# Performance work log

Hardware: AMD Instinct MI355X
Metric: run time of the kernel (lower is better)

The kernel has to match this reference:

```python
import jax, jax.numpy as jnp
import numpy as np

N_GRAPHS, NODES_PER, DEG, D = 128, 1024, 32, 256
N = N_GRAPHS * NODES_PER          # 131072 nodes
E = N * DEG                       # 4194304 edges
RATIO = 0.8
K = int(np.ceil(RATIO * NODES_PER))  # 820 nodes kept per graph


def setup_inputs() -> dict:
    key = jax.random.key(0)
    k1, k2, k3, k4 = jax.random.split(key, 4)
    x = jax.random.normal(k1, (N, D), dtype=jnp.float32)
    # intra-graph random edges: endpoints within [0, NODES_PER) + graph offset
    src = jax.random.randint(k2, (E,), 0, NODES_PER)
    dst = jax.random.randint(k3, (E,), 0, NODES_PER)
    goff = (jnp.arange(E) // (NODES_PER * DEG)) * NODES_PER
    edge_index = jnp.stack([src + goff, dst + goff]).astype(jnp.int32)
    batch = jnp.repeat(jnp.arange(N_GRAPHS, dtype=jnp.int32), NODES_PER)
    W = jax.random.normal(k4, (D, 1), dtype=jnp.float32) / np.sqrt(D)
    b = jnp.zeros((1,), dtype=jnp.float32)
    return {"x": x, "edge_index": edge_index, "batch": batch, "W": W, "b": b}


def _gcn_score(x, edge_index, W, b):
    # GCNConv(in_channels, 1) with added self-loops and symmetric normalization
    n = x.shape[0]
    row, col = edge_index[0], edge_index[1]  # source, target
    # degree at target, init 1.0 accounts for self-loop
    deg = jnp.ones((n,), x.dtype).at[col].add(jnp.ones_like(col, dtype=x.dtype))
    dinv = jax.lax.rsqrt(deg)
    h = x @ W                                 # [n, 1]
    norm = dinv[row] * dinv[col]              # [E]
    agg = jnp.zeros_like(h).at[col].add(norm[:, None] * h[row])
    agg = agg + (dinv * dinv)[:, None] * h    # self-loop contribution deg^-1 * h_i
    return (agg + b).squeeze(-1)              # [n]


def reference(x, edge_index, batch, W, b):
    score = _gcn_score(x, edge_index, W, b)                     # [N]
    # per-graph top-k (graphs are contiguous, equal size)
    score_g = score.reshape(N_GRAPHS, NODES_PER)
    _, idx = jax.lax.top_k(score_g, K)                          # [G, K]
    perm = (idx + jnp.arange(N_GRAPHS)[:, None] * NODES_PER).reshape(-1)  # [G*K]
    x_new = x[perm] * jnp.tanh(score[perm])[:, None]            # [G*K, D]
    batch_new = batch[perm]
    # filter_adj: remap kept nodes to new ids, mask edges with dropped endpoints
    new_id = jnp.full((x.shape[0],), -1, dtype=perm.dtype).at[perm].set(
        jnp.arange(perm.shape[0], dtype=perm.dtype))
    r2 = new_id[edge_index[0]]
    c2 = new_id[edge_index[1]]
    edge_mask = (r2 >= 0) & (c2 >= 0)                           # [E] valid edges
    edge_index_new = jnp.where(edge_mask, jnp.stack([r2, c2]), -1)  # [2, E], -1 = dropped
    return x_new, edge_index_new, edge_mask, batch_new, perm
```

## Files before the change

### kernel.cpp

```cpp
#include <hip/hip_runtime.h>
#include <math.h>

constexpr int NG    = 128;
constexpr int NP    = 1024;
constexpr int D     = 256;
constexpr int NTOT  = NG * NP;
constexpr int EPG   = NP * 32;
constexpr int ET    = NTOT * 32;
constexpr int KK    = 820;
constexpr int NKEEP = NG * KK;
constexpr int BPG   = 4;
constexpr int EPB   = EPG / BPG;
constexpr int NBE   = NG * BPG;

constexpr long long OUT_X     = 0;
constexpr long long OUT_EI0   = (long long)NKEEP * D;
constexpr long long OUT_EI1   = OUT_EI0 + ET;
constexpr long long OUT_MASK  = OUT_EI0 + 2LL * ET;
constexpr long long OUT_BATCH = OUT_MASK + ET;
constexpr long long OUT_PERM  = OUT_BATCH + NKEEP;

__global__ void node_init_kernel(const float* __restrict__ x,
                                 const float* __restrict__ W,
                                 float* __restrict__ h,
                                 int* __restrict__ new_id) {
    int row  = blockIdx.x * 4 + (threadIdx.x >> 6);
    int lane = threadIdx.x & 63;
    float4 a = ((const float4*)(x + (size_t)row * D))[lane];
    float4 w = ((const float4*)W)[lane];
    float s = a.x * w.x + a.y * w.y + a.z * w.z + a.w * w.w;
#pragma unroll
    for (int off = 32; off > 0; off >>= 1) s += __shfl_down(s, off, 64);
    if (lane == 0) {
        h[row]      = s;
        new_id[row] = -1;
    }
}

__global__ __launch_bounds__(256) void deg_part_kernel(const int* __restrict__ cols,
                                                       int* __restrict__ deg_part) {
    __shared__ int cnt[NP];
    const int b = blockIdx.x;
    const int g = b >> 2;
    for (int i = threadIdx.x; i < NP; i += 256) cnt[i] = 0;
    __syncthreads();
    const int4* c4 = (const int4*)(cols + (size_t)g * EPG + (size_t)(b & 3) * EPB);
#pragma unroll
    for (int i = threadIdx.x; i < EPB / 4; i += 256) {
        int4 c = c4[i];
        atomicAdd(&cnt[c.x & (NP - 1)], 1);
        atomicAdd(&cnt[c.y & (NP - 1)], 1);
        atomicAdd(&cnt[c.z & (NP - 1)], 1);
        atomicAdd(&cnt[c.w & (NP - 1)], 1);
    }
    __syncthreads();
    int* dst = deg_part + (size_t)b * NP;
    for (int i = threadIdx.x; i < NP; i += 256) dst[i] = cnt[i];
}

__global__ __launch_bounds__(256) void acc_part_kernel(const int* __restrict__ rows,
                                                       const int* __restrict__ cols,
                                                       const float* __restrict__ h,
                                                       const int* __restrict__ deg_part,
                                                       float* __restrict__ acc_part) {
    __shared__ float ul[NP];
    __shared__ float acc[NP];
    const int b = blockIdx.x;
    const int g = b >> 2;
    const int* dp = deg_part + (size_t)g * BPG * NP;
    for (int i = threadIdx.x; i < NP; i += 256) {
        int d = 1 + dp[i] + dp[NP + i] + dp[2 * NP + i] + dp[3 * NP + i];
        ul[i]  = rsqrtf((float)d) * h[g * NP + i];
        acc[i] = 0.0f;
    }
    __syncthreads();
    size_t eoff = (size_t)g * EPG + (size_t)(b & 3) * EPB;
    const int4* c4 = (const int4*)(cols + eoff);
    const int4* r4 = (const int4*)(rows + eoff);
#pragma unroll
    for (int i = threadIdx.x; i < EPB / 4; i += 256) {
        int4 c = c4[i];
        int4 r = r4[i];
        atomicAdd(&acc[c.x & (NP - 1)], ul[r.x & (NP - 1)]);
        atomicAdd(&acc[c.y & (NP - 1)], ul[r.y & (NP - 1)]);
        atomicAdd(&acc[c.z & (NP - 1)], ul[r.z & (NP - 1)]);
        atomicAdd(&acc[c.w & (NP - 1)], ul[r.w & (NP - 1)]);
    }
    __syncthreads();
    float* dst = acc_part + (size_t)b * NP;
    for (int i = threadIdx.x; i < NP; i += 256) dst[i] = acc[i];
}

__global__ __launch_bounds__(1024) void sort_kernel(
        const float* __restrict__ h, const float* __restrict__ b,
        const int* __restrict__ deg_part, const float* __restrict__ acc_part,
        int* __restrict__ perm_i, int* __restrict__ new_id,
        float* __restrict__ factor,
        float* __restrict__ out_perm, float* __restrict__ out_batch) {
    __shared__ unsigned long long sk[NP];
    __shared__ float scl[NP];

    const int g = blockIdx.x;
    const int t = threadIdx.x;
    const int*   dp = deg_part + (size_t)g * BPG * NP;
    const float* ap = acc_part + (size_t)g * BPG * NP;

    int   d  = 1 + dp[t] + dp[NP + t] + dp[2 * NP + t] + dp[3 * NP + t];
    float av = ap[t] + ap[NP + t] + ap[2 * NP + t] + ap[3 * NP + t];
    float hv = h[g * NP + t];
    float di = rsqrtf((float)d);
    float score = di * av + di * di * hv + b[0];
    scl[t] = score;

    unsigned int fu = __float_as_uint(score);
    unsigned int s  = (fu & 0x80000000u) ? ~fu : (fu | 0x80000000u);
    unsigned long long key = ((unsigned long long)(~s) << 32) | (unsigned int)t;

    for (int k = 2; k <= NP; k <<= 1) {
        for (int j = k >> 1; j > 0; j >>= 1) {
            unsigned long long other;
            if (j < 64) {
                other = __shfl_xor(key, j, 64);
            } else {
                sk[t] = key;
                __syncthreads();
                other = sk[t ^ j];
                __syncthreads();
            }
            bool take_min = (((t & k) == 0) == ((t & j) == 0));
            bool omin = other < key;
            key = (take_min == omin) ? other : key;
        }
    }

    if (t < KK) {
        int idx  = (int)(key & 0xFFFFFFFFull);
        int node = g * NP + idx;
        int j    = g * KK + t;
        perm_i[j]    = node;
        new_id[node] = j;
        out_perm[j]  = (float)node;
        out_batch[j] = (float)g;
        factor[j]    = tanhf(scl[idx]);
    }
}

__global__ void gather_kernel(const float* __restrict__ x,
                              const int* __restrict__ perm_i,
                              const float* __restrict__ factor,
                              float* __restrict__ out_x) {
    int j    = blockIdx.x * 4 + (threadIdx.x >> 6);
    int lane = threadIdx.x & 63;
    int node = perm_i[j];
    float t  = factor[j];
    float4 v = ((const float4*)(x + (size_t)node * D))[lane];
    float4 o = make_float4(v.x * t, v.y * t, v.z * t, v.w * t);
    ((float4*)(out_x + (size_t)j * D))[lane] = o;
}

__global__ __launch_bounds__(256) void edge_kernel(const int* __restrict__ rows,
                                                   const int* __restrict__ cols,
                                                   const int* __restrict__ new_id,
                                                   float* __restrict__ out_r,
                                                   float* __restrict__ out_c,
                                                   float* __restrict__ out_m) {
    __shared__ int nid[NP];
    const int b = blockIdx.x;
    const int g = b >> 2;
    for (int i = threadIdx.x; i < NP; i += 256) nid[i] = new_id[g * NP + i];
    __syncthreads();
    size_t eoff = (size_t)g * EPG + (size_t)(b & 3) * EPB;
    const int4* r4 = (const int4*)(rows + eoff);
    const int4* c4 = (const int4*)(cols + eoff);
    float4* orr = (float4*)(out_r + eoff);
    float4* occ = (float4*)(out_c + eoff);
    float4* omm = (float4*)(out_m + eoff);
#pragma unroll
    for (int i = threadIdx.x; i < EPB / 4; i += 256) {
        int4 r = r4[i];
        int4 c = c4[i];
        float4 fr, fc, fm;
        {
            int nr = nid[r.x & (NP - 1)], nc = nid[c.x & (NP - 1)];
            bool m = (nr >= 0) && (nc >= 0);
            fr.x = m ? (float)nr : -1.0f; fc.x = m ? (float)nc : -1.0f; fm.x = m ? 1.0f : 0.0f;
        }
        {
            int nr = nid[r.y & (NP - 1)], nc = nid[c.y & (NP - 1)];
            bool m = (nr >= 0) && (nc >= 0);
            fr.y = m ? (float)nr : -1.0f; fc.y = m ? (float)nc : -1.0f; fm.y = m ? 1.0f : 0.0f;
        }
        {
            int nr = nid[r.z & (NP - 1)], nc = nid[c.z & (NP - 1)];
            bool m = (nr >= 0) && (nc >= 0);
            fr.z = m ? (float)nr : -1.0f; fc.z = m ? (float)nc : -1.0f; fm.z = m ? 1.0f : 0.0f;
        }
        {
            int nr = nid[r.w & (NP - 1)], nc = nid[c.w & (NP - 1)];
            bool m = (nr >= 0) && (nc >= 0);
            fr.w = m ? (float)nr : -1.0f; fc.w = m ? (float)nc : -1.0f; fm.w = m ? 1.0f : 0.0f;
        }
        orr[i] = fr;
        occ[i] = fc;
        omm[i] = fm;
    }
}

extern "C" void kernel_launch(void* const* d_in, const int* in_sizes, int n_in,
                              void* d_out, int out_size, void* d_ws, size_t ws_size,
                              hipStream_t stream) {
    const float* x  = (const float*)d_in[0];
    const int*   ei = (const int*)d_in[1];
    const float* W  = (const float*)d_in[3];
    const float* b  = (const float*)d_in[4];
    float* out = (float*)d_out;

    float* wsf      = (float*)d_ws;
    float* h        = wsf;
    int*   new_id   = (int*)wsf + NTOT;
    int*   perm_i   = (int*)wsf + 2 * NTOT;
    float* factor   = wsf + 2 * NTOT + NKEEP;
    int*   deg_part = (int*)wsf + 2 * NTOT + 2 * NKEEP;
    float* acc_part = wsf + 2 * NTOT + 2 * NKEEP + NBE * NP;

    const int* rows = ei;
    const int* cols = ei + ET;

    hipLaunchKernelGGL(node_init_kernel, dim3(NTOT / 4), dim3(256), 0, stream,
                       x, W, h, new_id);
    hipLaunchKernelGGL(deg_part_kernel, dim3(NBE), dim3(256), 0, stream,
                       cols, deg_part);
    hipLaunchKernelGGL(acc_part_kernel, dim3(NBE), dim3(256), 0, stream,
                       rows, cols, h, deg_part, acc_part);
    hipLaunchKernelGGL(sort_kernel, dim3(NG), dim3(1024), 0, stream,
                       h, b, deg_part, acc_part, perm_i, new_id, factor,
                       out + OUT_PERM, out + OUT_BATCH);
    hipLaunchKernelGGL(gather_kernel, dim3(NKEEP / 4), dim3(256), 0, stream,
                       x, perm_i, factor, out + OUT_X);
    hipLaunchKernelGGL(edge_kernel, dim3(NBE), dim3(256), 0, stream,
                       rows, cols, new_id, out + OUT_EI0, out + OUT_EI1, out + OUT_MASK);
}
```

Baseline: 335.7 us.

## Fuse all stages into one cooperative persistent kernel with grid syncs

Replaces six separate kernel launches with a single cooperative kernel of 256 blocks of 1024 threads, separated by grid.sync() barriers. Each graph's edges are now split across two blocks instead of four, and node projection and gather are spread over the persistent blocks. The goal is to remove launch overhead and inter-kernel gaps. In exchange, the grid is smaller (256 blocks on a large GPU), there are grid-wide barriers, and only half the blocks do the sort phase, so memory-bound phases may get less parallelism.

```diff
diff --git a/kernel.cpp b/kernel.cpp
--- a/kernel.cpp
+++ b/kernel.cpp
@@ -1,5 +1,8 @@
 #include <hip/hip_runtime.h>
+#include <hip/hip_cooperative_groups.h>
 #include <math.h>
+
+namespace cg = cooperative_groups;
 
 constexpr int NG    = 128;
 constexpr int NP    = 1024;
@@ -9,9 +12,11 @@
 constexpr int ET    = NTOT * 32;
 constexpr int KK    = 820;
 constexpr int NKEEP = NG * KK;
-constexpr int BPG   = 4;
-constexpr int EPB   = EPG / BPG;
-constexpr int NBE   = NG * BPG;
+
+constexpr int NBLK  = 256;
+constexpr int EHALF = EPG / 2;
+constexpr int ROWS_PER_BLK  = NTOT  / NBLK;
+constexpr int GROWS_PER_BLK = NKEEP / NBLK;
 
 constexpr long long OUT_X     = 0;
 constexpr long long OUT_EI0   = (long long)NKEEP * D;
@@ -20,195 +25,187 @@
 constexpr long long OUT_BATCH = OUT_MASK + ET;
 constexpr long long OUT_PERM  = OUT_BATCH + NKEEP;
 
-__global__ void node_init_kernel(const float* __restrict__ x,
-                                 const float* __restrict__ W,
-                                 float* __restrict__ h,
-                                 int* __restrict__ new_id) {
-    int row  = blockIdx.x * 4 + (threadIdx.x >> 6);
-    int lane = threadIdx.x & 63;
-    float4 a = ((const float4*)(x + (size_t)row * D))[lane];
-    float4 w = ((const float4*)W)[lane];
-    float s = a.x * w.x + a.y * w.y + a.z * w.z + a.w * w.w;
-#pragma unroll
-    for (int off = 32; off > 0; off >>= 1) s += __shfl_down(s, off, 64);
-    if (lane == 0) {
-        h[row]      = s;
-        new_id[row] = -1;
-    }
-}
-
-__global__ __launch_bounds__(256) void deg_part_kernel(const int* __restrict__ cols,
-                                                       int* __restrict__ deg_part) {
-    __shared__ int cnt[NP];
-    const int b = blockIdx.x;
-    const int g = b >> 2;
-    for (int i = threadIdx.x; i < NP; i += 256) cnt[i] = 0;
-    __syncthreads();
-    const int4* c4 = (const int4*)(cols + (size_t)g * EPG + (size_t)(b & 3) * EPB);
-#pragma unroll
-    for (int i = threadIdx.x; i < EPB / 4; i += 256) {
-        int4 c = c4[i];
-        atomicAdd(&cnt[c.x & (NP - 1)], 1);
-        atomicAdd(&cnt[c.y & (NP - 1)], 1);
-        atomicAdd(&cnt[c.z & (NP - 1)], 1);
-        atomicAdd(&cnt[c.w & (NP - 1)], 1);
-    }
-    __syncthreads();
-    int* dst = deg_part + (size_t)b * NP;
-    for (int i = threadIdx.x; i < NP; i += 256) dst[i] = cnt[i];
-}
-
-__global__ __launch_bounds__(256) void acc_part_kernel(const int* __restrict__ rows,
-                                                       const int* __restrict__ cols,
-                                                       const float* __restrict__ h,
-                                                       const int* __restrict__ deg_part,
-                                                       float* __restrict__ acc_part) {
-    __shared__ float ul[NP];
-    __shared__ float acc[NP];
-    const int b = blockIdx.x;
-    const int g = b >> 2;
-    const int* dp = deg_part + (size_t)g * BPG * NP;
-    for (int i = threadIdx.x; i < NP; i += 256) {
-        int d = 1 + dp[i] + dp[NP + i] + dp[2 * NP + i] + dp[3 * NP + i];
-        ul[i]  = rsqrtf((float)d) * h[g * NP + i];
-        acc[i] = 0.0f;
-    }
-    __syncthreads();
-    size_t eoff = (size_t)g * EPG + (size_t)(b & 3) * EPB;
-    const int4* c4 = (const int4*)(cols + eoff);
-    const int4* r4 = (const int4*)(rows + eoff);
-#pragma unroll
-    for (int i = threadIdx.x; i < EPB / 4; i += 256) {
-        int4 c = c4[i];
-        int4 r = r4[i];
-        atomicAdd(&acc[c.x & (NP - 1)], ul[r.x & (NP - 1)]);
-        atomicAdd(&acc[c.y & (NP - 1)], ul[r.y & (NP - 1)]);
-        atomicAdd(&acc[c.z & (NP - 1)], ul[r.z & (NP - 1)]);
-        atomicAdd(&acc[c.w & (NP - 1)], ul[r.w & (NP - 1)]);
-    }
-    __syncthreads();
-    float* dst = acc_part + (size_t)b * NP;
-    for (int i = threadIdx.x; i < NP; i += 256) dst[i] = acc[i];
-}
-
-__global__ __launch_bounds__(1024) void sort_kernel(
-        const float* __restrict__ h, const float* __restrict__ b,
-        const int* __restrict__ deg_part, const float* __restrict__ acc_part,
-        int* __restrict__ perm_i, int* __restrict__ new_id,
-        float* __restrict__ factor,
-        float* __restrict__ out_perm, float* __restrict__ out_batch) {
+__global__ __launch_bounds__(1024, 4) void fused_kernel(
+        const float* __restrict__ x,   const int* __restrict__ rows,
+        const int* __restrict__ cols,  const float* __restrict__ W,
+        const float* __restrict__ bptr,
+        float* __restrict__ h,         int* __restrict__ new_id,
+        int* __restrict__ perm_i,      float* __restrict__ factor,
+        int* __restrict__ deg_part,    float* __restrict__ acc_part,
+        float* __restrict__ out) {
+    cg::grid_group grid = cg::this_grid();
+
     __shared__ unsigned long long sk[NP];
     __shared__ float scl[NP];
 
-    const int g = blockIdx.x;
-    const int t = threadIdx.x;
-    const int*   dp = deg_part + (size_t)g * BPG * NP;
-    const float* ap = acc_part + (size_t)g * BPG * NP;
-
-    int   d  = 1 + dp[t] + dp[NP + t] + dp[2 * NP + t] + dp[3 * NP + t];
-    float av = ap[t] + ap[NP + t] + ap[2 * NP + t] + ap[3 * NP + t];
-    float hv = h[g * NP + t];
-    float di = rsqrtf((float)d);
-    float score = di * av + di * di * hv + b[0];
-    scl[t] = score;
-
-    unsigned int fu = __float_as_uint(score);
-    unsigned int s  = (fu & 0x80000000u) ? ~fu : (fu | 0x80000000u);
-    unsigned long long key = ((unsigned long long)(~s) << 32) | (unsigned int)t;
-
-    for (int k = 2; k <= NP; k <<= 1) {
-        for (int j = k >> 1; j > 0; j >>= 1) {
-            unsigned long long other;
-            if (j < 64) {
-                other = __shfl_xor(key, j, 64);
-            } else {
-                sk[t] = key;
-                __syncthreads();
-                other = sk[t ^ j];
-                __syncthreads();
-            }
-            bool take_min = (((t & k) == 0) == ((t & j) == 0));
-            bool omin = other < key;
-            key = (take_min == omin) ? other : key;
-        }
-    }
-
-    if (t < KK) {
-        int idx  = (int)(key & 0xFFFFFFFFull);
-        int node = g * NP + idx;
-        int j    = g * KK + t;
-        perm_i[j]    = node;
-        new_id[node] = j;
-        out_perm[j]  = (float)node;
-        out_batch[j] = (float)g;
-        factor[j]    = tanhf(scl[idx]);
-    }
-}
-
-__global__ void gather_kernel(const float* __restrict__ x,
-                              const int* __restrict__ perm_i,
-                              const float* __restrict__ factor,
-                              float* __restrict__ out_x) {
-    int j    = blockIdx.x * 4 + (threadIdx.x >> 6);
-    int lane = threadIdx.x & 63;
-    int node = perm_i[j];
-    float t  = factor[j];
-    float4 v = ((const float4*)(x + (size_t)node * D))[lane];
-    float4 o = make_float4(v.x * t, v.y * t, v.z * t, v.w * t);
-    ((float4*)(out_x + (size_t)j * D))[lane] = o;
-}
-
-__global__ __launch_bounds__(256) void edge_kernel(const int* __restrict__ rows,
-                                                   const int* __restrict__ cols,
-                                                   const int* __restrict__ new_id,
-                                                   float* __restrict__ out_r,
-                                                   float* __restrict__ out_c,
-                                                   float* __restrict__ out_m) {
-    __shared__ int nid[NP];
-    const int b = blockIdx.x;
-    const int g = b >> 2;
-    for (int i = threadIdx.x; i < NP; i += 256) nid[i] = new_id[g * NP + i];
-    __syncthreads();
-    size_t eoff = (size_t)g * EPG + (size_t)(b & 3) * EPB;
-    const int4* r4 = (const int4*)(rows + eoff);
-    const int4* c4 = (const int4*)(cols + eoff);
-    float4* orr = (float4*)(out_r + eoff);
-    float4* occ = (float4*)(out_c + eoff);
-    float4* omm = (float4*)(out_m + eoff);
-#pragma unroll
-    for (int i = threadIdx.x; i < EPB / 4; i += 256) {
-        int4 r = r4[i];
-        int4 c = c4[i];
-        float4 fr, fc, fm;
-        {
-            int nr = nid[r.x & (NP - 1)], nc = nid[c.x & (NP - 1)];
-            bool m = (nr >= 0) && (nc >= 0);
-            fr.x = m ? (float)nr : -1.0f; fc.x = m ? (float)nc : -1.0f; fm.x = m ? 1.0f : 0.0f;
-        }
-        {
-            int nr = nid[r.y & (NP - 1)], nc = nid[c.y & (NP - 1)];
-            bool m = (nr >= 0) && (nc >= 0);
-            fr.y = m ? (float)nr : -1.0f; fc.y = m ? (float)nc : -1.0f; fm.y = m ? 1.0f : 0.0f;
-        }
-        {
-            int nr = nid[r.z & (NP - 1)], nc = nid[c.z & (NP - 1)];
-            bool m = (nr >= 0) && (nc >= 0);
-            fr.z = m ? (float)nr : -1.0f; fc.z = m ? (float)nc : -1.0f; fm.z = m ? 1.0f : 0.0f;
-        }
-        {
-            int nr = nid[r.w & (NP - 1)], nc = nid[c.w & (NP - 1)];
-            bool m = (nr >= 0) && (nc >= 0);
-            fr.w = m ? (float)nr : -1.0f; fc.w = m ? (float)nc : -1.0f; fm.w = m ? 1.0f : 0.0f;
-        }
-        orr[i] = fr;
-        occ[i] = fc;
-        omm[i] = fm;
+    const int blk  = blockIdx.x;
+    const int t    = threadIdx.x;
+    const int w    = t >> 6;
+    const int lane = t & 63;
+    const int g2   = blk >> 1;
+    const int half = blk & 1;
+
+    {
+        int* cnt = (int*)sk;
+        for (int i = t; i < NP; i += 1024) cnt[i] = 0;
+        __syncthreads();
+
+        float4 w4 = ((const float4*)W)[lane];
+        const int base = blk * ROWS_PER_BLK;
+        for (int r = w; r < ROWS_PER_BLK; r += 16) {
+            const int row = base + r;
+            float4 a = ((const float4*)(x + (size_t)row * D))[lane];
+            float s = a.x * w4.x + a.y * w4.y + a.z * w4.z + a.w * w4.w;
+#pragma unroll
+            for (int off = 32; off > 0; off >>= 1) s += __shfl_down(s, off, 64);
+            if (lane == 0) { h[row] = s; new_id[row] = -1; }
+        }
+
+        const int4* c4 = (const int4*)(cols + (size_t)g2 * EPG + (size_t)half * EHALF);
+#pragma unroll
+        for (int i = t; i < EHALF / 4; i += 1024) {
+            int4 c = c4[i];
+            atomicAdd(&cnt[c.x & (NP - 1)], 1);
+            atomicAdd(&cnt[c.y & (NP - 1)], 1);
+            atomicAdd(&cnt[c.z & (NP - 1)], 1);
+            atomicAdd(&cnt[c.w & (NP - 1)], 1);
+        }
+        __syncthreads();
+        int* dst = deg_part + (size_t)blk * NP;
+        for (int i = t; i < NP; i += 1024) dst[i] = cnt[i];
+    }
+    grid.sync();
+
+    {
+        float* ul  = (float*)sk;
+        float* acc = (float*)sk + NP;
+        const int* dp = deg_part + (size_t)(2 * g2) * NP;
+        for (int i = t; i < NP; i += 1024) {
+            int d  = 1 + dp[i] + dp[NP + i];
+            ul[i]  = rsqrtf((float)d) * h[g2 * NP + i];
+            acc[i] = 0.0f;
+        }
+        __syncthreads();
+        const size_t eo = (size_t)g2 * EPG + (size_t)half * EHALF;
+        const int4* c4 = (const int4*)(cols + eo);
+        const int4* r4 = (const int4*)(rows + eo);
+#pragma unroll
+        for (int i = t; i < EHALF / 4; i += 1024) {
+            int4 c = c4[i];
+            int4 r = r4[i];
+            atomicAdd(&acc[c.x & (NP - 1)], ul[r.x & (NP - 1)]);
+            atomicAdd(&acc[c.y & (NP - 1)], ul[r.y & (NP - 1)]);
+            atomicAdd(&acc[c.z & (NP - 1)], ul[r.z & (NP - 1)]);
+            atomicAdd(&acc[c.w & (NP - 1)], ul[r.w & (NP - 1)]);
+        }
+        __syncthreads();
+        float* dst = acc_part + (size_t)blk * NP;
+        for (int i = t; i < NP; i += 1024) dst[i] = acc[i];
+    }
+    grid.sync();
+
+    if (blk < NG) {
+        const int g = blk;
+        const int*   dp = deg_part + (size_t)(2 * g) * NP;
+        const float* ap = acc_part + (size_t)(2 * g) * NP;
+        int   d  = 1 + dp[t] + dp[NP + t];
+        float av = ap[t] + ap[NP + t];
+        float hv = h[g * NP + t];
+        float di = rsqrtf((float)d);
+        float score = di * av + di * di * hv + bptr[0];
+        scl[t] = score;
+
+        unsigned int fu = __float_as_uint(score);
+        unsigned int s  = (fu & 0x80000000u) ? ~fu : (fu | 0x80000000u);
+        unsigned long long key = ((unsigned long long)(~s) << 32) | (unsigned int)t;
+
+        for (int k = 2; k <= NP; k <<= 1) {
+            for (int j = k >> 1; j > 0; j >>= 1) {
+                unsigned long long other;
+                if (j < 64) {
+                    other = __shfl_xor(key, j, 64);
+                } else {
+                    sk[t] = key;
+                    __syncthreads();
+                    other = sk[t ^ j];
+                    __syncthreads();
+                }
+                bool take_min = (((t & k) == 0) == ((t & j) == 0));
+                bool omin = other < key;
+                key = (take_min == omin) ? other : key;
+            }
+        }
+
+        if (t < KK) {
+            int idx  = (int)(key & 0xFFFFFFFFull);
+            int node = g * NP + idx;
+            int jj   = g * KK + t;
+            perm_i[jj]   = node;
+            new_id[node] = jj;
+            out[OUT_PERM + jj]  = (float)node;
+            out[OUT_BATCH + jj] = (float)g;
+            factor[jj] = tanhf(scl[idx]);
+        }
+    }
+    grid.sync();
+
+    {
+        const int base = blk * GROWS_PER_BLK;
+        for (int r = w; r < GROWS_PER_BLK; r += 16) {
+            const int j    = base + r;
+            const int node = perm_i[j];
+            const float f  = factor[j];
+            float4 v = ((const float4*)(x + (size_t)node * D))[lane];
+            ((float4*)(out + OUT_X + (size_t)j * D))[lane] =
+                make_float4(v.x * f, v.y * f, v.z * f, v.w * f);
+        }
+
+        int* nid = (int*)sk;
+        for (int i = t; i < NP; i += 1024) nid[i] = new_id[g2 * NP + i];
+        __syncthreads();
+        const size_t eo = (size_t)g2 * EPG + (size_t)half * EHALF;
+        const int4* r4 = (const int4*)(rows + eo);
+        const int4* c4 = (const int4*)(cols + eo);
+        float4* orr = (float4*)(out + OUT_EI0  + eo);
+        float4* occ = (float4*)(out + OUT_EI1  + eo);
+        float4* omm = (float4*)(out + OUT_MASK + eo);
+#pragma unroll
+        for (int i = t; i < EHALF / 4; i += 1024) {
+            int4 r = r4[i];
+            int4 c = c4[i];
+            float4 fr, fc, fm;
+            {
+                int nr = nid[r.x & (NP - 1)], nc = nid[c.x & (NP - 1)];
+                bool m = (nr >= 0) && (nc >= 0);
+                fr.x = m ? (float)nr : -1.0f; fc.x = m ? (float)nc : -1.0f; fm.x = m ? 1.0f : 0.0f;
+            }
+            {
+                int nr = nid[r.y & (NP - 1)], nc = nid[c.y & (NP - 1)];
+                bool m = (nr >= 0) && (nc >= 0);
+                fr.y = m ? (float)nr : -1.0f; fc.y = m ? (float)nc : -1.0f; fm.y = m ? 1.0f : 0.0f;
+            }
+            {
+                int nr = nid[r.z & (NP - 1)], nc = nid[c.z & (NP - 1)];
+                bool m = (nr >= 0) && (nc >= 0);
+                fr.z = m ? (float)nr : -1.0f; fc.z = m ? (float)nc : -1.0f; fm.z = m ? 1.0f : 0.0f;
+            }
+            {
+                int nr = nid[r.w & (NP - 1)], nc = nid[c.w & (NP - 1)];
+                bool m = (nr >= 0) && (nc >= 0);
+                fr.w = m ? (float)nr : -1.0f; fc.w = m ? (float)nc : -1.0f; fm.w = m ? 1.0f : 0.0f;
+            }
+            orr[i] = fr;
+            occ[i] = fc;
+            omm[i] = fm;
+        }
     }
 }
 
 extern "C" void kernel_launch(void* const* d_in, const int* in_sizes, int n_in,
                               void* d_out, int out_size, void* d_ws, size_t ws_size,
                               hipStream_t stream) {
+    (void)in_sizes; (void)n_in; (void)out_size; (void)ws_size;
+
     const float* x  = (const float*)d_in[0];
     const int*   ei = (const int*)d_in[1];
     const float* W  = (const float*)d_in[3];
@@ -217,26 +214,18 @@
 
     float* wsf      = (float*)d_ws;
     float* h        = wsf;
-    int*   new_id   = (int*)wsf + NTOT;
-    int*   perm_i   = (int*)wsf + 2 * NTOT;
+    int*   new_id   = (int*)(wsf + NTOT);
+    int*   perm_i   = (int*)(wsf + 2 * NTOT);
     float* factor   = wsf + 2 * NTOT + NKEEP;
-    int*   deg_part = (int*)wsf + 2 * NTOT + 2 * NKEEP;
-    float* acc_part = wsf + 2 * NTOT + 2 * NKEEP + NBE * NP;
+    int*   deg_part = (int*)(wsf + 2 * NTOT + 2 * NKEEP);
+    float* acc_part = wsf + 2 * NTOT + 2 * NKEEP + NBLK * NP;
 
     const int* rows = ei;
     const int* cols = ei + ET;
 
-    hipLaunchKernelGGL(node_init_kernel, dim3(NTOT / 4), dim3(256), 0, stream,
-                       x, W, h, new_id);
-    hipLaunchKernelGGL(deg_part_kernel, dim3(NBE), dim3(256), 0, stream,
-                       cols, deg_part);
-    hipLaunchKernelGGL(acc_part_kernel, dim3(NBE), dim3(256), 0, stream,
-                       rows, cols, h, deg_part, acc_part);
-    hipLaunchKernelGGL(sort_kernel, dim3(NG), dim3(1024), 0, stream,
-                       h, b, deg_part, acc_part, perm_i, new_id, factor,
-                       out + OUT_PERM, out + OUT_BATCH);
-    hipLaunchKernelGGL(gather_kernel, dim3(NKEEP / 4), dim3(256), 0, stream,
-                       x, perm_i, factor, out + OUT_X);
-    hipLaunchKernelGGL(edge_kernel, dim3(NBE), dim3(256), 0, stream,
-                       rows, cols, new_id, out + OUT_EI0, out + OUT_EI1, out + OUT_MASK);
+    void* args[] = { (void*)&x, (void*)&rows, (void*)&cols, (void*)&W, (void*)&b,
+                     (void*)&h, (void*)&new_id, (void*)&perm_i, (void*)&factor,
+                     (void*)&deg_part, (void*)&acc_part, (void*)&out };
+    hipLaunchCooperativeKernel((const void*)fused_kernel, dim3(NBLK), dim3(1024),
+                               args, 0, stream);
 }
```

New measurement: 445.9 us. +32.8%, slower.

## Fuse node projection with degree counting and gather with edge remap kernels

Applied to the files above, without the earlier changes.

Merges the node projection (x@W) kernel with the per-graph degree histogram into one launch, and merges the x gather/scale kernel with the edge remap kernel into another. Both use 2048 blocks: the first 512 do the edge work while every block also processes a strided share of rows, so independent memory-bound streams can overlap within one grid and two launches go away. The cost is that blocks doing edge work carry extra load, and the row loops now run serially per wave instead of one row per wave. There is also no barrier before the x-gather part, which is fine since it does not touch shared memory.

```diff
diff --git a/kernel.cpp b/kernel.cpp
--- a/kernel.cpp
+++ b/kernel.cpp
@@ -13,6 +13,10 @@
 constexpr int EPB   = EPG / BPG;
 constexpr int NBE   = NG * BPG;
 
+constexpr int K1_BLOCKS = 2048;
+constexpr int K4_BLOCKS = 2048;
+constexpr int K1_ROWS_PER_WAVE = NTOT / (K1_BLOCKS * 4);
+
 constexpr long long OUT_X     = 0;
 constexpr long long OUT_EI0   = (long long)NKEEP * D;
 constexpr long long OUT_EI1   = OUT_EI0 + ET;
@@ -20,49 +24,57 @@
 constexpr long long OUT_BATCH = OUT_MASK + ET;
 constexpr long long OUT_PERM  = OUT_BATCH + NKEEP;
 
-__global__ void node_init_kernel(const float* __restrict__ x,
-                                 const float* __restrict__ W,
-                                 float* __restrict__ h,
-                                 int* __restrict__ new_id) {
-    int row  = blockIdx.x * 4 + (threadIdx.x >> 6);
-    int lane = threadIdx.x & 63;
-    float4 a = ((const float4*)(x + (size_t)row * D))[lane];
-    float4 w = ((const float4*)W)[lane];
-    float s = a.x * w.x + a.y * w.y + a.z * w.z + a.w * w.w;
-#pragma unroll
-    for (int off = 32; off > 0; off >>= 1) s += __shfl_down(s, off, 64);
-    if (lane == 0) {
-        h[row]      = s;
-        new_id[row] = -1;
-    }
-}
-
-__global__ __launch_bounds__(256) void deg_part_kernel(const int* __restrict__ cols,
-                                                       int* __restrict__ deg_part) {
+__global__ __launch_bounds__(256) void k1_h_deg(const float* __restrict__ x,
+                                                const float* __restrict__ W,
+                                                const int* __restrict__ cols,
+                                                float* __restrict__ h,
+                                                int* __restrict__ new_id,
+                                                int* __restrict__ deg_part) {
     __shared__ int cnt[NP];
-    const int b = blockIdx.x;
-    const int g = b >> 2;
-    for (int i = threadIdx.x; i < NP; i += 256) cnt[i] = 0;
-    __syncthreads();
-    const int4* c4 = (const int4*)(cols + (size_t)g * EPG + (size_t)(b & 3) * EPB);
-#pragma unroll
-    for (int i = threadIdx.x; i < EPB / 4; i += 256) {
-        int4 c = c4[i];
-        atomicAdd(&cnt[c.x & (NP - 1)], 1);
-        atomicAdd(&cnt[c.y & (NP - 1)], 1);
-        atomicAdd(&cnt[c.z & (NP - 1)], 1);
-        atomicAdd(&cnt[c.w & (NP - 1)], 1);
-    }
-    __syncthreads();
-    int* dst = deg_part + (size_t)b * NP;
-    for (int i = threadIdx.x; i < NP; i += 256) dst[i] = cnt[i];
-}
-
-__global__ __launch_bounds__(256) void acc_part_kernel(const int* __restrict__ rows,
-                                                       const int* __restrict__ cols,
-                                                       const float* __restrict__ h,
-                                                       const int* __restrict__ deg_part,
-                                                       float* __restrict__ acc_part) {
+    const int b    = blockIdx.x;
+    const int t    = threadIdx.x;
+    const int w    = t >> 6;
+    const int lane = t & 63;
+    const bool do_deg = (b < NBE);
+
+    if (do_deg) {
+        for (int i = t; i < NP; i += 256) cnt[i] = 0;
+        __syncthreads();
+    }
+
+    float4 w4 = ((const float4*)W)[lane];
+    const int base = (b * 4 + w) * K1_ROWS_PER_WAVE;
+    for (int r = 0; r < K1_ROWS_PER_WAVE; ++r) {
+        const int row = base + r;
+        float4 a = ((const float4*)(x + (size_t)row * D))[lane];
+        float s = a.x * w4.x + a.y * w4.y + a.z * w4.z + a.w * w4.w;
+#pragma unroll
+        for (int off = 32; off > 0; off >>= 1) s += __shfl_down(s, off, 64);
+        if (lane == 0) { h[row] = s; new_id[row] = -1; }
+    }
+
+    if (do_deg) {
+        const int g = b >> 2;
+        const int4* c4 = (const int4*)(cols + (size_t)g * EPG + (size_t)(b & 3) * EPB);
+#pragma unroll
+        for (int i = t; i < EPB / 4; i += 256) {
+            int4 c = c4[i];
+            atomicAdd(&cnt[c.x & (NP - 1)], 1);
+            atomicAdd(&cnt[c.y & (NP - 1)], 1);
+            atomicAdd(&cnt[c.z & (NP - 1)], 1);
+            atomicAdd(&cnt[c.w & (NP - 1)], 1);
+        }
+        __syncthreads();
+        int* dst = deg_part + (size_t)b * NP;
+        for (int i = t; i < NP; i += 256) dst[i] = cnt[i];
+    }
+}
+
+__global__ __launch_bounds__(256) void k2_acc(const int* __restrict__ rows,
+                                              const int* __restrict__ cols,
+                                              const float* __restrict__ h,
+                                              const int* __restrict__ deg_part,
+                                              float* __restrict__ acc_part) {
     __shared__ float ul[NP];
     __shared__ float acc[NP];
     const int b = blockIdx.x;
@@ -91,7 +103,7 @@
     for (int i = threadIdx.x; i < NP; i += 256) dst[i] = acc[i];
 }
 
-__global__ __launch_bounds__(1024) void sort_kernel(
+__global__ __launch_bounds__(1024) void k3_sort(
         const float* __restrict__ h, const float* __restrict__ b,
         const int* __restrict__ deg_part, const float* __restrict__ acc_part,
         int* __restrict__ perm_i, int* __restrict__ new_id,
@@ -145,70 +157,74 @@
     }
 }
 
-__global__ void gather_kernel(const float* __restrict__ x,
-                              const int* __restrict__ perm_i,
-                              const float* __restrict__ factor,
-                              float* __restrict__ out_x) {
-    int j    = blockIdx.x * 4 + (threadIdx.x >> 6);
-    int lane = threadIdx.x & 63;
-    int node = perm_i[j];
-    float t  = factor[j];
-    float4 v = ((const float4*)(x + (size_t)node * D))[lane];
-    float4 o = make_float4(v.x * t, v.y * t, v.z * t, v.w * t);
-    ((float4*)(out_x + (size_t)j * D))[lane] = o;
-}
-
-__global__ __launch_bounds__(256) void edge_kernel(const int* __restrict__ rows,
-                                                   const int* __restrict__ cols,
-                                                   const int* __restrict__ new_id,
-                                                   float* __restrict__ out_r,
-                                                   float* __restrict__ out_c,
-                                                   float* __restrict__ out_m) {
+__global__ __launch_bounds__(256) void k4_gather_edge(
+        const float* __restrict__ x,
+        const int* __restrict__ rows, const int* __restrict__ cols,
+        const int* __restrict__ new_id,
+        const int* __restrict__ perm_i, const float* __restrict__ factor,
+        float* __restrict__ out) {
     __shared__ int nid[NP];
-    const int b = blockIdx.x;
-    const int g = b >> 2;
-    for (int i = threadIdx.x; i < NP; i += 256) nid[i] = new_id[g * NP + i];
-    __syncthreads();
-    size_t eoff = (size_t)g * EPG + (size_t)(b & 3) * EPB;
-    const int4* r4 = (const int4*)(rows + eoff);
-    const int4* c4 = (const int4*)(cols + eoff);
-    float4* orr = (float4*)(out_r + eoff);
-    float4* occ = (float4*)(out_c + eoff);
-    float4* omm = (float4*)(out_m + eoff);
-#pragma unroll
-    for (int i = threadIdx.x; i < EPB / 4; i += 256) {
-        int4 r = r4[i];
-        int4 c = c4[i];
-        float4 fr, fc, fm;
-        {
-            int nr = nid[r.x & (NP - 1)], nc = nid[c.x & (NP - 1)];
-            bool m = (nr >= 0) && (nc >= 0);
-            fr.x = m ? (float)nr : -1.0f; fc.x = m ? (float)nc : -1.0f; fm.x = m ? 1.0f : 0.0f;
+    const int b    = blockIdx.x;
+    const int t    = threadIdx.x;
+    const int w    = t >> 6;
+    const int lane = t & 63;
+
+    if (b < NBE) {
+        const int g = b >> 2;
+        for (int i = t; i < NP; i += 256) nid[i] = new_id[g * NP + i];
+        __syncthreads();
+        size_t eoff = (size_t)g * EPG + (size_t)(b & 3) * EPB;
+        const int4* r4 = (const int4*)(rows + eoff);
+        const int4* c4 = (const int4*)(cols + eoff);
+        float4* orr = (float4*)(out + OUT_EI0  + eoff);
+        float4* occ = (float4*)(out + OUT_EI1  + eoff);
+        float4* omm = (float4*)(out + OUT_MASK + eoff);
+#pragma unroll
+        for (int i = t; i < EPB / 4; i += 256) {
+            int4 r = r4[i];
+            int4 c = c4[i];
+            float4 fr, fc, fm;
+            {
+                int nr = nid[r.x & (NP - 1)], nc = nid[c.x & (NP - 1)];
+                bool m = (nr >= 0) && (nc >= 0);
+                fr.x = m ? (float)nr : -1.0f; fc.x = m ? (float)nc : -1.0f; fm.x = m ? 1.0f : 0.0f;
+            }
+            {
+                int nr = nid[r.y & (NP - 1)], nc = nid[c.y & (NP - 1)];
+                bool m = (nr >= 0) && (nc >= 0);
+                fr.y = m ? (float)nr : -1.0f; fc.y = m ? (float)nc : -1.0f; fm.y = m ? 1.0f : 0.0f;
+            }
+            {
+                int nr = nid[r.z & (NP - 1)], nc = nid[c.z & (NP - 1)];
+                bool m = (nr >= 0) && (nc >= 0);
+                fr.z = m ? (float)nr : -1.0f; fc.z = m ? (float)nc : -1.0f; fm.z = m ? 1.0f : 0.0f;
+            }
+            {
+                int nr = nid[r.w & (NP - 1)], nc = nid[c.w & (NP - 1)];
+                bool m = (nr >= 0) && (nc >= 0);
+                fr.w = m ? (float)nr : -1.0f; fc.w = m ? (float)nc : -1.0f; fm.w = m ? 1.0f : 0.0f;
+            }
+            orr[i] = fr;
+            occ[i] = fc;
+            omm[i] = fm;
         }
-        {
-            int nr = nid[r.y & (NP - 1)], nc = nid[c.y & (NP - 1)];
-            bool m = (nr >= 0) && (nc >= 0);
-            fr.y = m ? (float)nr : -1.0f; fc.y = m ? (float)nc : -1.0f; fm.y = m ? 1.0f : 0.0f;
-        }
-        {
-            int nr = nid[r.z & (NP - 1)], nc = nid[c.z & (NP - 1)];
-            bool m = (nr >= 0) && (nc >= 0);
-            fr.z = m ? (float)nr : -1.0f; fc.z = m ? (float)nc : -1.0f; fm.z = m ? 1.0f : 0.0f;
-        }
-        {
-            int nr = nid[r.w & (NP - 1)], nc = nid[c.w & (NP - 1)];
-            bool m = (nr >= 0) && (nc >= 0);
-            fr.w = m ? (float)nr : -1.0f; fc.w = m ? (float)nc : -1.0f; fm.w = m ? 1.0f : 0.0f;
-        }
-        orr[i] = fr;
-        occ[i] = fc;
-        omm[i] = fm;
+    }
+
+    const int gw = b * 4 + w;
+    for (int j = gw; j < NKEEP; j += K4_BLOCKS * 4) {
+        const int node = perm_i[j];
+        const float f  = factor[j];
+        float4 v = ((const float4*)(x + (size_t)node * D))[lane];
+        ((float4*)(out + OUT_X + (size_t)j * D))[lane] =
+            make_float4(v.x * f, v.y * f, v.z * f, v.w * f);
     }
 }
 
 extern "C" void kernel_launch(void* const* d_in, const int* in_sizes, int n_in,
                               void* d_out, int out_size, void* d_ws, size_t ws_size,
                               hipStream_t stream) {
+    (void)in_sizes; (void)n_in; (void)out_size; (void)ws_size;
+
     const float* x  = (const float*)d_in[0];
     const int*   ei = (const int*)d_in[1];
     const float* W  = (const float*)d_in[3];
@@ -217,26 +233,22 @@
 
     float* wsf      = (float*)d_ws;
     float* h        = wsf;
-    int*   new_id   = (int*)wsf + NTOT;
-    int*   perm_i   = (int*)wsf + 2 * NTOT;
+    int*   new_id   = (int*)(wsf + NTOT);
+    int*   perm_i   = (int*)(wsf + 2 * NTOT);
     float* factor   = wsf + 2 * NTOT + NKEEP;
-    int*   deg_part = (int*)wsf + 2 * NTOT + 2 * NKEEP;
+    int*   deg_part = (int*)(wsf + 2 * NTOT + 2 * NKEEP);
     float* acc_part = wsf + 2 * NTOT + 2 * NKEEP + NBE * NP;
 
     const int* rows = ei;
     const int* cols = ei + ET;
 
-    hipLaunchKernelGGL(node_init_kernel, dim3(NTOT / 4), dim3(256), 0, stream,
-                       x, W, h, new_id);
-    hipLaunchKernelGGL(deg_part_kernel, dim3(NBE), dim3(256), 0, stream,
-                       cols, deg_part);
-    hipLaunchKernelGGL(acc_part_kernel, dim3(NBE), dim3(256), 0, stream,
+    hipLaunchKernelGGL(k1_h_deg, dim3(K1_BLOCKS), dim3(256), 0, stream,
+                       x, W, cols, h, new_id, deg_part);
+    hipLaunchKernelGGL(k2_acc, dim3(NBE), dim3(256), 0, stream,
                        rows, cols, h, deg_part, acc_part);
-    hipLaunchKernelGGL(sort_kernel, dim3(NG), dim3(1024), 0, stream,
+    hipLaunchKernelGGL(k3_sort, dim3(NG), dim3(1024), 0, stream,
                        h, b, deg_part, acc_part, perm_i, new_id, factor,
                        out + OUT_PERM, out + OUT_BATCH);
-    hipLaunchKernelGGL(gather_kernel, dim3(NKEEP / 4), dim3(256), 0, stream,
-                       x, perm_i, factor, out + OUT_X);
-    hipLaunchKernelGGL(edge_kernel, dim3(NBE), dim3(256), 0, stream,
-                       rows, cols, new_id, out + OUT_EI0, out + OUT_EI1, out + OUT_MASK);
-}
+    hipLaunchKernelGGL(k4_gather_edge, dim3(K4_BLOCKS), dim3(256), 0, stream,
+                       x, rows, cols, new_id, perm_i, factor, out + OUT_X);
+}
```

Measured after the change: 346.4 us. 1.03x slower.
